# Kernel tuning notes

Measured on AMD Instinct MI355X. Metric: run time of the kernel, lower is better.

Reference implementation:

```python
import jax, jax.numpy as jnp
import numpy as np

EPS = 1e-3  # matches module default eps=0.001


def setup_inputs() -> dict:
    key = jax.random.key(0)
    k1, k2 = jax.random.split(key)
    B, C, W, H = 8, 64, 496, 432  # KITTI BEV grid, pillar feature dim 64
    x = jax.random.normal(k1, (B, C, W, H), dtype=jnp.float32)
    # are exactly zero across all channels so x.sum(1) == 0 there.
    occ = (jax.random.uniform(k2, (B, W, H)) < 0.10).astype(jnp.float32)
    x = x * occ[:, None, :, :]
    return {"x": x}


def reference(x):
    # Faithful to the torch module, including its padding artifact: each batch's
    # nonzero index list is padded to N = max(num_nonzeros) with index (0,0), so
    # padded slots gather x[b,:,0,0], contribute to mean/var with multiplicity
    # (N - n_b), and scatter a normalized value back into pixel (0,0).
    B, C, Wd, Hd = x.shape
    mask = (x.sum(axis=1) != 0)                 # [B,W,H] occupied pixels
    n = mask.sum(axis=(1, 2))                    # [B] nonzeros per batch
    N = n.max()                                  # padded gather length
    pad = (N - n).astype(x.dtype)                # [B] number of (0,0) pad slots
    x00 = x[:, :, 0, 0]                          # [B,C] value gathered by pads
    mb = mask[:, None, :, :].astype(x.dtype)     # [B,1,W,H]

    count = (B * N).astype(x.dtype)              # total gathered entries
    total = (x * mb).sum(axis=(0, 2, 3)) + (pad[:, None] * x00).sum(axis=0)  # [C]
    mean = total / count                         # [C]

    d = x - mean[None, :, None, None]
    sq = ((d * d) * mb).sum(axis=(0, 2, 3)) + (pad[:, None] * (x00 - mean) ** 2).sum(axis=0)
    var = sq / count                             # [C] biased variance (mean over gathered)

    inv = 1.0 / jnp.sqrt(var + EPS)              # [C]; note: mean is NOT subtracted
    out = jnp.where(mask[:, None, :, :], x * inv[None, :, None, None], x)

    # scatter-back hits (0,0) whenever batch b had pad slots OR (0,0) was nonzero
    write00 = (pad > 0) | mask[:, 0, 0]          # [B]
    out = out.at[:, :, 0, 0].set(
        jnp.where(write00[:, None], x00 * inv[None, :], out[:, :, 0, 0])
    )
    return out
```

## Files before the change

### kernel.cpp

```cpp
#include <hip/hip_runtime.h>

#define WH      214272
#define GPB     53568
#define NGROUP  (8*GPB)
#define TOTAL4  (512*GPB)

#define STATS_BLOCKS 1024
#define SCALE_BLOCKS 2048

typedef float floatx4 __attribute__((ext_vector_type(4)));

__global__ __launch_bounds__(256, 4) void k_stats(const floatx4* __restrict__ x4,
                                                  float* __restrict__ gsum,
                                                  float* __restrict__ gsq,
                                                  int* __restrict__ gn) {
    const int tid  = threadIdx.x;
    const int lane = tid & 63;
    const int wave = tid >> 6;
    const int c0   = wave * 16;

    float acc[16];
    float acc2[16];
#pragma unroll
    for (int j = 0; j < 16; ++j) { acc[j] = 0.f; acc2[j] = 0.f; }

    const int stride = STATS_BLOCKS * 64;
    for (int i = blockIdx.x * 64 + lane; i < NGROUP; i += stride) {
        const int b = (int)((unsigned)i / GPB);
        const int r = i - b * GPB;
        const floatx4* p = x4 + (size_t)(b * 64 + c0) * GPB + r;
        float sx = 0.f, sy = 0.f, sz = 0.f, sw = 0.f;
#pragma unroll
        for (int j = 0; j < 16; ++j) {
            const floatx4 v = p[(size_t)j * GPB];
            sx += v.x; sy += v.y; sz += v.z; sw += v.w;
            acc[j] += (v.x + v.y) + (v.z + v.w);
            acc2[j] = fmaf(v.w, v.w, fmaf(v.z, v.z, fmaf(v.y, v.y, fmaf(v.x, v.x, acc2[j]))));
        }
        if (wave == 0) {
            int cnt = (sx != 0.f) + (sy != 0.f) + (sz != 0.f) + (sw != 0.f);
#pragma unroll
            for (int m = 1; m < 64; m <<= 1) cnt += __shfl_xor(cnt, m, 64);
            if (lane == 0) atomicAdd(&gn[b], cnt);
        }
    }

    float mysum = 0.f, mysq = 0.f;
#pragma unroll
    for (int j = 0; j < 16; ++j) {
        float r1 = acc[j], r2 = acc2[j];
#pragma unroll
        for (int m = 1; m < 64; m <<= 1) {
            r1 += __shfl_xor(r1, m, 64);
            r2 += __shfl_xor(r2, m, 64);
        }
        if (lane == j) { mysum = r1; mysq = r2; }
    }
    if (lane < 16) {
        atomicAdd(&gsum[c0 + lane], mysum);
        atomicAdd(&gsq[c0 + lane], mysq);
    }
}

__global__ __launch_bounds__(256, 8) void k_scale(const floatx4* __restrict__ x4,
                                                  floatx4* __restrict__ out4,
                                                  const float* __restrict__ gsum,
                                                  const float* __restrict__ gsq,
                                                  const int* __restrict__ gn) {
    __shared__ float sinv[64];
    const int tid = threadIdx.x;
    if (tid < 64) {
        const int c = tid;
        const float* x = (const float*)x4;
        int nb[8];
        int N = 0;
#pragma unroll
        for (int b = 0; b < 8; ++b) { nb[b] = gn[b]; N = max(N, nb[b]); }
        float total = gsum[c];
        float S2    = gsq[c];
#pragma unroll
        for (int b = 0; b < 8; ++b) {
            const float pad = (float)(N - nb[b]);
            const float x00 = x[(size_t)(b * 64 + c) * WH];
            total = fmaf(pad, x00, total);
            S2    = fmaf(pad, x00 * x00, S2);
        }
        const float count = (float)(8 * N);
        const float mean  = total / count;
        const float var   = S2 / count - mean * mean;
        sinv[c] = 1.0f / sqrtf(var + 0.001f);
    }
    __syncthreads();

    const int nthreads = SCALE_BLOCKS * 256;
    for (int i = blockIdx.x * 256 + tid; i < TOTAL4; i += nthreads) {
        const int plane = (int)((unsigned)i / GPB);
        const float inv = sinv[plane & 63];
        floatx4 v = x4[i];
        v.x *= inv; v.y *= inv; v.z *= inv; v.w *= inv;
        __builtin_nontemporal_store(v, &out4[i]);
    }
}

extern "C" void kernel_launch(void* const* d_in, const int* in_sizes, int n_in,
                              void* d_out, int out_size, void* d_ws, size_t ws_size,
                              hipStream_t stream) {
    const float* x  = (const float*)d_in[0];
    float* out      = (float*)d_out;
    float* wsf      = (float*)d_ws;
    float* gsum     = wsf;
    float* gsq      = wsf + 64;
    int*   gn       = (int*)(wsf + 128);

    (void)hipMemsetAsync(d_ws, 0, 136 * sizeof(float), stream);

    k_stats<<<STATS_BLOCKS, 256, 0, stream>>>((const floatx4*)x, gsum, gsq, gn);
    k_scale<<<SCALE_BLOCKS, 256, 0, stream>>>((const floatx4*)x, (floatx4*)out,
                                              gsum, gsq, gn);
}
```

Measured before the change: 796.4 us.

## Stream contiguous per-wave chunks in stats and reverse-order nontemporal scale pass

The stats kernel now gives each wave a contiguous range of 1KB chunks within a plane, instead of strided 16-channel gathers across planes. It accumulates the sum and sum of squares per plane and counts nonzeros only on channel 0. The scale kernel walks chunks in reverse order so its first reads hit data the stats pass touched last and may still be cached, and it uses nontemporal loads. The cost is more atomics per plane segment, and the reverse-order reuse depends on how much of x stays in L2 or the MALL.

```diff
diff --git a/kernel.cpp b/kernel.cpp
--- a/kernel.cpp
+++ b/kernel.cpp
@@ -2,8 +2,9 @@
 
 #define WH      214272
 #define GPB     53568
-#define NGROUP  (8*GPB)
 #define TOTAL4  (512*GPB)
+#define CHUNKS  (TOTAL4/64)
+#define CPP     (GPB/64)
 
 #define STATS_BLOCKS 1024
 #define SCALE_BLOCKS 2048
@@ -14,51 +15,44 @@
                                                   float* __restrict__ gsum,
                                                   float* __restrict__ gsq,
                                                   int* __restrict__ gn) {
-    const int tid  = threadIdx.x;
-    const int lane = tid & 63;
-    const int wave = tid >> 6;
-    const int c0   = wave * 16;
+    const int lane = threadIdx.x & 63;
+    const int gw   = blockIdx.x * 4 + (threadIdx.x >> 6);
+    const int nw   = STATS_BLOCKS * 4;
+    const int per  = (CHUNKS + nw - 1) / nw;
+    int c0 = gw * per;
+    const int c1 = min(c0 + per, CHUNKS);
 
-    float acc[16];
-    float acc2[16];
+    while (c0 < c1) {
+        const int plane = (int)((unsigned)c0 / CPP);
+        const int run   = min(c1, (plane + 1) * CPP);
+        const bool isC0 = (plane & 63) == 0;
+
+        float s = 0.f, q = 0.f;
+        int cnt = 0;
+        const floatx4* p = x4 + (size_t)c0 * 64 + lane;
+        const int n = run - c0;
+#pragma unroll 4
+        for (int k = 0; k < n; ++k) {
+            const floatx4 v = p[(size_t)k * 64];
+            s += (v.x + v.y) + (v.z + v.w);
+            q = fmaf(v.w, v.w, fmaf(v.z, v.z, fmaf(v.y, v.y, fmaf(v.x, v.x, q))));
+            if (isC0) cnt += (v.x != 0.f) + (v.y != 0.f) + (v.z != 0.f) + (v.w != 0.f);
+        }
 #pragma unroll
-    for (int j = 0; j < 16; ++j) { acc[j] = 0.f; acc2[j] = 0.f; }
-
-    const int stride = STATS_BLOCKS * 64;
-    for (int i = blockIdx.x * 64 + lane; i < NGROUP; i += stride) {
-        const int b = (int)((unsigned)i / GPB);
-        const int r = i - b * GPB;
-        const floatx4* p = x4 + (size_t)(b * 64 + c0) * GPB + r;
-        float sx = 0.f, sy = 0.f, sz = 0.f, sw = 0.f;
-#pragma unroll
-        for (int j = 0; j < 16; ++j) {
-            const floatx4 v = p[(size_t)j * GPB];
-            sx += v.x; sy += v.y; sz += v.z; sw += v.w;
-            acc[j] += (v.x + v.y) + (v.z + v.w);
-            acc2[j] = fmaf(v.w, v.w, fmaf(v.z, v.z, fmaf(v.y, v.y, fmaf(v.x, v.x, acc2[j]))));
+        for (int m = 1; m < 64; m <<= 1) {
+            s += __shfl_xor(s, m, 64);
+            q += __shfl_xor(q, m, 64);
         }
-        if (wave == 0) {
-            int cnt = (sx != 0.f) + (sy != 0.f) + (sz != 0.f) + (sw != 0.f);
+        if (isC0) {
 #pragma unroll
             for (int m = 1; m < 64; m <<= 1) cnt += __shfl_xor(cnt, m, 64);
-            if (lane == 0) atomicAdd(&gn[b], cnt);
         }
-    }
-
-    float mysum = 0.f, mysq = 0.f;
-#pragma unroll
-    for (int j = 0; j < 16; ++j) {
-        float r1 = acc[j], r2 = acc2[j];
-#pragma unroll
-        for (int m = 1; m < 64; m <<= 1) {
-            r1 += __shfl_xor(r1, m, 64);
-            r2 += __shfl_xor(r2, m, 64);
+        if (lane == 0) {
+            atomicAdd(&gsum[plane & 63], s);
+            atomicAdd(&gsq[plane & 63], q);
+            if (isC0) atomicAdd(&gn[plane >> 6], cnt);
         }
-        if (lane == j) { mysum = r1; mysq = r2; }
-    }
-    if (lane < 16) {
-        atomicAdd(&gsum[c0 + lane], mysum);
-        atomicAdd(&gsq[c0 + lane], mysq);
+        c0 = run;
     }
 }
 
@@ -92,11 +86,15 @@
     }
     __syncthreads();
 
-    const int nthreads = SCALE_BLOCKS * 256;
-    for (int i = blockIdx.x * 256 + tid; i < TOTAL4; i += nthreads) {
-        const int plane = (int)((unsigned)i / GPB);
+    const int lane = tid & 63;
+    const int gw   = blockIdx.x * 4 + (tid >> 6);
+    const int nw   = SCALE_BLOCKS * 4;
+#pragma unroll 2
+    for (int ch = CHUNKS - 1 - gw; ch >= 0; ch -= nw) {
+        const int plane = (int)((unsigned)ch / CPP);
         const float inv = sinv[plane & 63];
-        floatx4 v = x4[i];
+        const size_t i = (size_t)ch * 64 + lane;
+        floatx4 v = __builtin_nontemporal_load(&x4[i]);
         v.x *= inv; v.y *= inv; v.z *= inv; v.w *= inv;
         __builtin_nontemporal_store(v, &out4[i]);
     }
```

Result: no change. 791.8 us (-0.6%).
